# Kernel tuning notes

Measured on AMD Instinct MI355X. Metric: run time of the kernel, lower is better.

The kernel has to match this reference:

```python
import jax, jax.numpy as jnp
import numpy as np

BATCH = 16384
FEAT = 2048
NUM_CLASSES = 1000


def setup_inputs() -> dict:
    key = jax.random.key(0)
    k1, k2, k3 = jax.random.split(key, 3)
    x = jax.random.normal(k1, (BATCH, FEAT), dtype=jnp.float32)
    labels = jax.random.randint(k2, (BATCH,), 0, NUM_CLASSES, dtype=jnp.int64)
    centers = jax.random.normal(k3, (NUM_CLASSES, FEAT), dtype=jnp.float32)
    return {"x": x, "labels": labels, "centers": centers}


def reference(x, labels, centers):
    # Vectorized gather + squared-diff + full reduction (the torch loop fused).
    diff = x - centers[labels]                      # (B, F)
    loss = jnp.sum(diff * diff)                     # scalar
    batch_size = x.shape[0]
    return loss / 2.0 / batch_size
```

## Files before the change

kernel.cpp:

```cpp
#include <hip/hip_runtime.h>
#include <hip/hip_bf16.h>


#define CL_BATCH 16384
#define CL_FEAT  2048
#define CL_F4    (CL_FEAT / 4)
#define CL_NBLK  2048
#define CL_TPB   256

__global__ __launch_bounds__(CL_TPB) void center_loss_partial_kernel(
    const float* __restrict__ x,
    const int* __restrict__ labels,
    const float* __restrict__ centers,
    float* __restrict__ partial) {
  const int total4 = CL_BATCH * CL_F4;
  const float4* __restrict__ x4 = reinterpret_cast<const float4*>(x);
  const float4* __restrict__ c4 = reinterpret_cast<const float4*>(centers);

  float acc = 0.0f;
  int stride = gridDim.x * blockDim.x;
  for (int f = blockIdx.x * blockDim.x + threadIdx.x; f < total4; f += stride) {
    int row  = f >> 9;
    int col4 = f & 511;
    int lab  = labels[row];
    float4 xv = x4[f];
    float4 cv = c4[lab * CL_F4 + col4];
    float dx = xv.x - cv.x;
    float dy = xv.y - cv.y;
    float dz = xv.z - cv.z;
    float dw = xv.w - cv.w;
    acc += dx * dx + dy * dy + dz * dz + dw * dw;
  }

  #pragma unroll
  for (int off = 32; off > 0; off >>= 1)
    acc += __shfl_down(acc, off, 64);

  __shared__ float lds[CL_TPB / 64];
  int wave = threadIdx.x >> 6;
  int lane = threadIdx.x & 63;
  if (lane == 0) lds[wave] = acc;
  __syncthreads();
  if (threadIdx.x == 0) {
    float s = 0.0f;
    #pragma unroll
    for (int w = 0; w < CL_TPB / 64; ++w) s += lds[w];
    partial[blockIdx.x] = s;
  }
}

__global__ __launch_bounds__(CL_TPB) void center_loss_reduce_kernel(
    const float* __restrict__ partial, float* __restrict__ out) {
  float acc = 0.0f;
  for (int i = threadIdx.x; i < CL_NBLK; i += CL_TPB) acc += partial[i];
  #pragma unroll
  for (int off = 32; off > 0; off >>= 1)
    acc += __shfl_down(acc, off, 64);

  __shared__ float lds[CL_TPB / 64];
  int wave = threadIdx.x >> 6;
  int lane = threadIdx.x & 63;
  if (lane == 0) lds[wave] = acc;
  __syncthreads();
  if (threadIdx.x == 0) {
    float s = 0.0f;
    #pragma unroll
    for (int w = 0; w < CL_TPB / 64; ++w) s += lds[w];
    out[0] = s * (0.5f / (float)CL_BATCH);
  }
}

extern "C" void kernel_launch(void* const* d_in, const int* in_sizes, int n_in,
                              void* d_out, int out_size, void* d_ws, size_t ws_size,
                              hipStream_t stream) {
  const float* x       = (const float*)d_in[0];
  const int*   labels  = (const int*)d_in[1];
  const float* centers = (const float*)d_in[2];
  float* out     = (float*)d_out;
  float* partial = (float*)d_ws;

  center_loss_partial_kernel<<<CL_NBLK, CL_TPB, 0, stream>>>(x, labels, centers, partial);
  center_loss_reduce_kernel<<<1, CL_TPB, 0, stream>>>(partial, out);
}
```

Measured before the change: 194.8 us.

## Assign fixed rows per block with hoisted labels and nontemporal x loads

Replaces the grid-stride loop with a fixed mapping: each 512-thread block handles 8 full rows, and each thread reads one float4 per row. The labels for those rows are loaded up front and the loop is fully unrolled, so 8 independent loads are in flight per thread and there is no per-element label load or index math. x is read with nontemporal loads so the streamed data does not evict the reused centers from cache. The cost is 2048 blocks with exactly one pass each, so there is no tail amortization, and register pressure goes up.

```diff
diff --git a/kernel.cpp b/kernel.cpp
--- a/kernel.cpp
+++ b/kernel.cpp
@@ -4,32 +4,35 @@
 
 #define CL_BATCH 16384
 #define CL_FEAT  2048
-#define CL_F4    (CL_FEAT / 4)
-#define CL_NBLK  2048
-#define CL_TPB   256
+#define CL_F4    512
+#define CL_TPB   512
+#define CL_RPB   8
+#define CL_NBLK  (CL_BATCH / CL_RPB)
+
+typedef float f32x4 __attribute__((ext_vector_type(4)));
 
 __global__ __launch_bounds__(CL_TPB) void center_loss_partial_kernel(
     const float* __restrict__ x,
     const int* __restrict__ labels,
     const float* __restrict__ centers,
     float* __restrict__ partial) {
-  const int total4 = CL_BATCH * CL_F4;
-  const float4* __restrict__ x4 = reinterpret_cast<const float4*>(x);
-  const float4* __restrict__ c4 = reinterpret_cast<const float4*>(centers);
+  const f32x4* __restrict__ x4 = reinterpret_cast<const f32x4*>(x);
+  const f32x4* __restrict__ c4 = reinterpret_cast<const f32x4*>(centers);
+
+  const int r0 = blockIdx.x * CL_RPB;
+  const int t  = threadIdx.x;
+
+  int lab[CL_RPB];
+  #pragma unroll
+  for (int k = 0; k < CL_RPB; ++k) lab[k] = labels[r0 + k];
 
   float acc = 0.0f;
-  int stride = gridDim.x * blockDim.x;
-  for (int f = blockIdx.x * blockDim.x + threadIdx.x; f < total4; f += stride) {
-    int row  = f >> 9;
-    int col4 = f & 511;
-    int lab  = labels[row];
-    float4 xv = x4[f];
-    float4 cv = c4[lab * CL_F4 + col4];
-    float dx = xv.x - cv.x;
-    float dy = xv.y - cv.y;
-    float dz = xv.z - cv.z;
-    float dw = xv.w - cv.w;
-    acc += dx * dx + dy * dy + dz * dz + dw * dw;
+  #pragma unroll
+  for (int k = 0; k < CL_RPB; ++k) {
+    f32x4 xv = __builtin_nontemporal_load(&x4[(size_t)(r0 + k) * CL_F4 + t]);
+    f32x4 cv = c4[(size_t)lab[k] * CL_F4 + t];
+    f32x4 d = xv - cv;
+    acc += d.x * d.x + d.y * d.y + d.z * d.z + d.w * d.w;
   }
 
   #pragma unroll
@@ -49,15 +52,15 @@
   }
 }
 
-__global__ __launch_bounds__(CL_TPB) void center_loss_reduce_kernel(
+__global__ __launch_bounds__(256) void center_loss_reduce_kernel(
     const float* __restrict__ partial, float* __restrict__ out) {
   float acc = 0.0f;
-  for (int i = threadIdx.x; i < CL_NBLK; i += CL_TPB) acc += partial[i];
+  for (int i = threadIdx.x; i < CL_NBLK; i += 256) acc += partial[i];
   #pragma unroll
   for (int off = 32; off > 0; off >>= 1)
     acc += __shfl_down(acc, off, 64);
 
-  __shared__ float lds[CL_TPB / 64];
+  __shared__ float lds[4];
   int wave = threadIdx.x >> 6;
   int lane = threadIdx.x & 63;
   if (lane == 0) lds[wave] = acc;
@@ -65,7 +68,7 @@
   if (threadIdx.x == 0) {
     float s = 0.0f;
     #pragma unroll
-    for (int w = 0; w < CL_TPB / 64; ++w) s += lds[w];
+    for (int w = 0; w < 4; ++w) s += lds[w];
     out[0] = s * (0.5f / (float)CL_BATCH);
   }
 }
@@ -80,5 +83,5 @@
   float* partial = (float*)d_ws;
 
   center_loss_partial_kernel<<<CL_NBLK, CL_TPB, 0, stream>>>(x, labels, centers, partial);
-  center_loss_reduce_kernel<<<1, CL_TPB, 0, stream>>>(partial, out);
+  center_loss_reduce_kernel<<<1, 256, 0, stream>>>(partial, out);
 }
```

New measurement: 197.2 us. No clear change (+1.2%).
